# Kernel tuning notes

Measured on AMD Instinct MI355X. Metric: run time of the kernel, lower is better.

The kernel has to match this reference:

```python
import jax, jax.numpy as jnp
import numpy as np

NUM_GROUPS = 64  # matches fill_max of ids; all groups present w.h.p. so unique-inverse == ids


def setup_inputs() -> dict:
    key = jax.random.key(0)
    ks = jax.random.split(key, 8)
    B, N, D = 8, 8192, 512
    s = 1.0 / np.sqrt(D)
    return {
        "x": jax.random.normal(ks[0], (B, N, D), dtype=jnp.float32),
        "ids": jax.random.randint(ks[1], (N,), 0, NUM_GROUPS),
        "w1": jax.random.normal(ks[2], (D, D), dtype=jnp.float32) * s,
        "b1": jax.random.normal(ks[3], (D,), dtype=jnp.float32) * s,
        "w2": jax.random.normal(ks[4], (D, D), dtype=jnp.float32) * s,
        "b2": jax.random.normal(ks[5], (D,), dtype=jnp.float32) * s,
        "w3": jax.random.normal(ks[6], (D, D), dtype=jnp.float32) * s,
        "b3": jax.random.normal(ks[7], (D,), dtype=jnp.float32) * s,
    }


def reference(x, ids, w1, b1, w2, b2, w3, b3):
    # x: [B, N, D]; ids: [N] group labels in [0, NUM_GROUPS)
    G = NUM_GROUPS
    a = jnp.einsum('bnd,ed->bne', x, w1) + b1          # linear1 logits
    v = jnp.einsum('bnd,ed->bne', x, w2) + b2          # linear2 values
    # move segment axis to front: [N, B, D]
    aT = jnp.transpose(a, (1, 0, 2))
    vT = jnp.transpose(v, (1, 0, 2))
    # per-group stable softmax along the segment axis
    mx = jax.lax.stop_gradient(jax.ops.segment_max(aT, ids, num_segments=G))  # [G,B,D]
    ex = jnp.exp(aT - mx[ids])
    denom = jax.ops.segment_sum(ex, ids, num_segments=G)                      # [G,B,D]
    wts = ex / denom[ids]                                                     # [N,B,D]
    # weighted scatter-sum of values -> [G, B, D] -> [B, G, D]
    y = jnp.transpose(jax.ops.segment_sum(vT * wts, ids, num_segments=G), (1, 0, 2))
    out = jnp.einsum('bgd,ed->bge', y, w3) + b3        # linear3
    # expand: gather group outputs back to per-element rows -> [B, N, D]
    return out[:, ids]
```

## Files before the change

kernel.cpp:

```cpp
#include <hip/hip_runtime.h>
#include <hip/hip_bf16.h>
#include <math.h>

#define B_ 8
#define N_ 8192
#define D_ 512
#define G_ 64
#define M_ (B_ * N_)

typedef short bf16x8 __attribute__((ext_vector_type(8)));
typedef float f32x4 __attribute__((ext_vector_type(4)));

__device__ __forceinline__ unsigned short f2bf(float f) {
    __hip_bfloat16 h = __float2bfloat16(f);
    return *reinterpret_cast<unsigned short*>(&h);
}
__device__ __forceinline__ void gload_lds16(const void* g, void* l) {
    __builtin_amdgcn_global_load_lds((const __attribute__((address_space(1))) void*)g,
                                     (__attribute__((address_space(3))) void*)l,
                                     16, 0, 0);
}

__global__ __launch_bounds__(256) void cast_x(const float* __restrict__ x,
                                              unsigned short* __restrict__ xb) {
    size_t t = (size_t)blockIdx.x * 256 + threadIdx.x;
    float4 f = *(const float4*)(x + t * 4);
    ushort4 u;
    u.x = f2bf(f.x); u.y = f2bf(f.y); u.z = f2bf(f.z); u.w = f2bf(f.w);
    *(ushort4*)(xb + t * 4) = u;
}

__global__ __launch_bounds__(256) void cast_w(const float* __restrict__ w1,
                                              const float* __restrict__ b1,
                                              const float* __restrict__ w2,
                                              const float* __restrict__ b2,
                                              unsigned short* __restrict__ wB,
                                              float* __restrict__ biasB) {
    int t = blockIdx.x * 256 + threadIdx.x;
    int idx = t * 4;
    int row = idx >> 9;
    int col = idx & 511;
    const float* src = (row < 512) ? (w1 + (size_t)row * 512 + col)
                                   : (w2 + (size_t)(row - 512) * 512 + col);
    float4 f = *(const float4*)src;
    ushort4 u;
    u.x = f2bf(f.x); u.y = f2bf(f.y); u.z = f2bf(f.z); u.w = f2bf(f.w);
    *(ushort4*)(wB + idx) = u;
    if (t < 1024) biasB[t] = (t < 512) ? b1[t] : b2[t - 512];
}

__global__ __launch_bounds__(256) void build_lists3(const int* __restrict__ ids,
                                                    int* __restrict__ counts,
                                                    int* __restrict__ baseO,
                                                    int* __restrict__ fgO,
                                                    int* __restrict__ perm) {
    __shared__ int sid[N_];
    __shared__ unsigned short hist[256][G_];
    __shared__ int sbase[G_ + 1];
    const int t = threadIdx.x;
    for (int i = t; i < N_; i += 256) sid[i] = ids[i];
#pragma unroll
    for (int g = 0; g < G_; ++g) hist[t][g] = 0;
    __syncthreads();
    const int nb = t * 32;
    for (int k = 0; k < 32; ++k) hist[t][sid[nb + k]]++;
    __syncthreads();
    if (t < G_) {
        int run = 0;
        for (int i = 0; i < 256; ++i) {
            int v = hist[i][t];
            hist[i][t] = (unsigned short)run;
            run += v;
        }
        counts[t] = run;
    }
    __syncthreads();
    if (t == 0) {
        int acc = 0;
        for (int g = 0; g < G_; ++g) { sbase[g] = acc; acc += counts[g]; }
        sbase[G_] = acc;
    }
    __syncthreads();
    if (t < G_) baseO[t] = sbase[t];
    if (t < G_) {
        const int row = t * 128;
        int g = 0;
        while (g + 1 < G_ && sbase[g + 1] <= row) ++g;
        fgO[t] = g;
    }
    for (int k = 0; k < 32; ++k) {
        const int n = nb + k;
        const int g = sid[n];
        const int pos = sbase[g] + hist[t][g];
        hist[t][g]++;
        perm[pos] = n;
    }
}

__global__ __launch_bounds__(256) void gemm_fused(const unsigned short* __restrict__ xb,
                                                  const unsigned short* __restrict__ wB,
                                                  const float* __restrict__ biasB,
                                                  const int* __restrict__ perm,
                                                  const int* __restrict__ base,
                                                  const int* __restrict__ fg,
                                                  float* __restrict__ pt) {
    __shared__ unsigned short lsA[2][128 * 64];
    __shared__ unsigned short lsB[2][2][64 * 64];

    const int o  = blockIdx.x;
    const int mt = (o & 7) + ((o >> 6) << 3);
    const int et = (o >> 3) & 7;
    const int b  = mt >> 6;
    const int tl = mt & 63;
    const int r0 = tl * 128;

    const int tid = threadIdx.x;
    const int l = tid & 63;
    const int w = tid >> 6;
    const int wm = w >> 1, wn = w & 1;
    const int lr = l >> 3;
    const int lslot = l & 7;
    const int fr = l & 15;
    const int scol = 8 * (lslot ^ lr);

    int nrow[4];
#pragma unroll
    for (int q = 0; q < 4; ++q) nrow[q] = perm[r0 + (w * 4 + q) * 8 + lr];

    f32x4 acc_a[4][2], acc_v[4][2];
#pragma unroll
    for (int i = 0; i < 4; ++i)
#pragma unroll
        for (int j = 0; j < 2; ++j) {
            acc_a[i][j] = (f32x4){0.f, 0.f, 0.f, 0.f};
            acc_v[i][j] = (f32x4){0.f, 0.f, 0.f, 0.f};
        }

    auto stageT = [&](int buf, int kt) {
#pragma unroll
        for (int q = 0; q < 4; ++q) {
            const int c = w * 4 + q;
            gload_lds16(xb + (((size_t)(b << 13) + nrow[q]) << 9) + kt + scol,
                        &lsA[buf][c * 512]);
        }
#pragma unroll
        for (int q = 0; q < 4; ++q) {
            const int p = q >> 1;
            const int c2 = (w << 1) | (q & 1);
            const int wr = p * 512 + et * 64 + c2 * 8 + lr;
            gload_lds16(wB + ((size_t)wr << 9) + kt + scol, &lsB[buf][p][c2 * 512]);
        }
    };

    stageT(0, 0);
    __syncthreads();
    int cur = 0;
    for (int t = 0; t < 8; ++t) {
        if (t < 7) stageT(cur ^ 1, (t + 1) * 64);
#pragma unroll
        for (int ks = 0; ks < 2; ++ks) {
            const int ib = 8 * ((ks * 4 + (l >> 4)) ^ (fr & 7));
            bf16x8 af[4], bq[2][2];
#pragma unroll
            for (int i = 0; i < 4; ++i)
                af[i] = *(const bf16x8*)&lsA[cur][(wm * 64 + i * 16 + fr) * 64 + ib];
#pragma unroll
            for (int p = 0; p < 2; ++p)
#pragma unroll
                for (int j = 0; j < 2; ++j)
                    bq[p][j] = *(const bf16x8*)&lsB[cur][p][(wn * 32 + j * 16 + fr) * 64 + ib];
#pragma unroll
            for (int i = 0; i < 4; ++i)
#pragma unroll
                for (int j = 0; j < 2; ++j) {
                    acc_a[i][j] = __builtin_amdgcn_mfma_f32_16x16x32_bf16(af[i], bq[0][j], acc_a[i][j], 0, 0, 0);
                    acc_v[i][j] = __builtin_amdgcn_mfma_f32_16x16x32_bf16(af[i], bq[1][j], acc_v[i][j], 0, 0, 0);
                }
        }
        __syncthreads();
        cur ^= 1;
    }

    const int fg0 = fg[tl];
    const int bnd0 = (fg0 + 1 < G_) ? base[fg0 + 1] : (1 << 30);
    const int bnd1 = (fg0 + 2 < G_) ? base[fg0 + 2] : (1 << 30);
    const int bnd2 = (fg0 + 3 < G_) ? base[fg0 + 3] : (1 << 30);
    float b1c[2], b2c[2];
#pragma unroll
    for (int j = 0; j < 2; ++j) {
        const int col = et * 64 + wn * 32 + j * 16 + fr;
        b1c[j] = biasB[col];
        b2c[j] = biasB[512 + col];
    }
    float dpart[4][2] = {}, ypart[4][2] = {};
    const int rbase = r0 + wm * 64 + ((l >> 4) << 2);
#pragma unroll
    for (int i = 0; i < 4; ++i)
#pragma unroll
        for (int rr = 0; rr < 4; ++rr) {
            const int row = rbase + i * 16 + rr;
            const int s = (row >= bnd0) + (row >= bnd1) + (row >= bnd2);
#pragma unroll
            for (int j = 0; j < 2; ++j) {
                const float e = __expf(acc_a[i][j][rr] + b1c[j]);
                const float ey = e * (acc_v[i][j][rr] + b2c[j]);
#pragma unroll
                for (int s2 = 0; s2 < 4; ++s2) {
                    dpart[s2][j] += (s == s2) ? e : 0.f;
                    ypart[s2][j] += (s == s2) ? ey : 0.f;
                }
            }
        }
#pragma unroll
    for (int s2 = 0; s2 < 4; ++s2)
#pragma unroll
        for (int j = 0; j < 2; ++j) {
            dpart[s2][j] += __shfl_xor(dpart[s2][j], 16);
            dpart[s2][j] += __shfl_xor(dpart[s2][j], 32);
            ypart[s2][j] += __shfl_xor(ypart[s2][j], 16);
            ypart[s2][j] += __shfl_xor(ypart[s2][j], 32);
        }
    float* red = (float*)&lsA[0][0];
    if ((l >> 4) == 0) {
#pragma unroll
        for (int s2 = 0; s2 < 4; ++s2)
#pragma unroll
            for (int j = 0; j < 2; ++j) {
                const int colL = wn * 32 + j * 16 + fr;
                red[((wm * 4 + s2) * 64 + colL) * 2 + 0] = dpart[s2][j];
                red[((wm * 4 + s2) * 64 + colL) * 2 + 1] = ypart[s2][j];
            }
    }
    __syncthreads();
#pragma unroll
    for (int k = 0; k < 2; ++k) {
        const int idx = tid * 2 + k;
        const int dy = idx & 1;
        const int colL = (idx >> 1) & 63;
        const int s2 = idx >> 7;
        const float vsum = red[((0 * 4 + s2) * 64 + colL) * 2 + dy] +
                           red[((1 * 4 + s2) * 64 + colL) * 2 + dy];
        pt[((((size_t)(b * 64 + tl)) * 4 + s2) * 512 + et * 64 + colL) * 2 + dy] = vsum;
    }
}

__global__ __launch_bounds__(256) void combineC(const float* __restrict__ pt,
                                                const int* __restrict__ base,
                                                const int* __restrict__ counts,
                                                const int* __restrict__ fg,
                                                float* __restrict__ y) {
    const int g = blockIdx.x, b = blockIdx.y;
    const int bs = base[g];
    int cnt = counts[g];
    if (cnt == 0) cnt = 1;
    const int t0 = bs >> 7, t1 = (bs + cnt - 1) >> 7;
    for (int c = threadIdx.x; c < 512; c += 256) {
        float d = 0.f, yy = 0.f;
        for (int t = t0; t <= t1; ++t) {
            const int s = g - fg[t];
            if (s >= 0 && s < 4) {
                const float* p = &pt[((((size_t)(b * 64 + t)) * 4 + s) * 512 + c) * 2];
                d += p[0];
                yy += p[1];
            }
        }
        y[((size_t)(b * G_ + g)) * 512 + c] = yy / d;
    }
}

__global__ __launch_bounds__(256) void gemm3(const float* __restrict__ y,
                                             const float* __restrict__ w3,
                                             const float* __restrict__ b3,
                                             float* __restrict__ out_small) {
    __shared__ float ys[16][68];
    __shared__ float wss[16][68];
    const int m0 = blockIdx.x * 64;
    const int n0 = blockIdx.y * 64;
    const int tid = threadIdx.x;
    const int tr = tid >> 4;
    const int tc = tid & 15;
    const int lrow = tid >> 2;
    const int lk4 = (tid & 3) * 4;

    float acc[4][4] = {};

    for (int k0 = 0; k0 < D_; k0 += 16) {
        float4 yv = *(const float4*)(y + (size_t)(m0 + lrow) * D_ + k0 + lk4);
        float4 wv = *(const float4*)(w3 + (size_t)(n0 + lrow) * D_ + k0 + lk4);
        __syncthreads();
        ys[lk4 + 0][lrow] = yv.x;  ys[lk4 + 1][lrow] = yv.y;
        ys[lk4 + 2][lrow] = yv.z;  ys[lk4 + 3][lrow] = yv.w;
        wss[lk4 + 0][lrow] = wv.x; wss[lk4 + 1][lrow] = wv.y;
        wss[lk4 + 2][lrow] = wv.z; wss[lk4 + 3][lrow] = wv.w;
        __syncthreads();
#pragma unroll
        for (int kk = 0; kk < 16; ++kk) {
            float4 y4 = *(const float4*)&ys[kk][tr * 4];
            float4 w4 = *(const float4*)&wss[kk][tc * 4];
            float ya[4] = {y4.x, y4.y, y4.z, y4.w};
            float wa[4] = {w4.x, w4.y, w4.z, w4.w};
#pragma unroll
            for (int i = 0; i < 4; ++i)
#pragma unroll
                for (int j = 0; j < 4; ++j)
                    acc[i][j] = fmaf(ya[i], wa[j], acc[i][j]);
        }
    }

    float bb[4];
#pragma unroll
    for (int j = 0; j < 4; ++j) bb[j] = b3[n0 + tc * 4 + j];
#pragma unroll
    for (int i = 0; i < 4; ++i) {
        size_t o = (size_t)(m0 + tr * 4 + i) * D_ + n0 + tc * 4;
        float4 r;
        r.x = acc[i][0] + bb[0]; r.y = acc[i][1] + bb[1];
        r.z = acc[i][2] + bb[2]; r.w = acc[i][3] + bb[3];
        *(float4*)(out_small + o) = r;
    }
}

__global__ __launch_bounds__(256) void gather_out(const int* __restrict__ ids,
                                                  const float* __restrict__ out_small,
                                                  float* __restrict__ out) {
    const int c = blockIdx.x * 256 + threadIdx.x;
    const int per_row = D_ / 4;
    const int b = c / (N_ * per_row);
    const int rem = c % (N_ * per_row);
    const int n = rem / per_row;
    const int q = rem % per_row;
    const int g = ids[n];
    float4 val = *(const float4*)(out_small + ((size_t)b * G_ + g) * D_ + q * 4);
    *(float4*)(out + (size_t)c * 4) = val;
}

extern "C" void kernel_launch(void* const* d_in, const int* in_sizes, int n_in,
                              void* d_out, int out_size, void* d_ws, size_t ws_size,
                              hipStream_t stream) {
    (void)in_sizes; (void)n_in; (void)out_size; (void)ws_size;
    const float* x   = (const float*)d_in[0];
    const int*   ids = (const int*)d_in[1];
    const float* w1  = (const float*)d_in[2];
    const float* b1  = (const float*)d_in[3];
    const float* w2  = (const float*)d_in[4];
    const float* b2  = (const float*)d_in[5];
    const float* w3  = (const float*)d_in[6];
    const float* b3  = (const float*)d_in[7];
    float* out = (float*)d_out;

    float* ws_f = (float*)d_ws;
    unsigned short* xb = (unsigned short*)ws_f;
    float* after_xb  = ws_f + 16777216;
    unsigned short* wB = (unsigned short*)after_xb;
    float* biasB     = after_xb + 262144;
    float* pt        = biasB + 1024;
    float* y         = pt + 2097152;
    float* out_small = y + 262144;
    int*   perm      = (int*)(out_small + 262144);
    int*   base      = perm + N_;
    int*   counts    = base + G_;
    int*   fg        = counts + G_;

    hipLaunchKernelGGL(cast_x, dim3(32768), dim3(256), 0, stream, x, xb);
    hipLaunchKernelGGL(cast_w, dim3(512), dim3(256), 0, stream, w1, b1, w2, b2, wB, biasB);
    hipLaunchKernelGGL(build_lists3, dim3(1), dim3(256), 0, stream, ids, counts, base, fg, perm);
    hipLaunchKernelGGL(gemm_fused, dim3(4096), dim3(256), 0, stream,
                       xb, wB, biasB, perm, base, fg, pt);
    hipLaunchKernelGGL(combineC, dim3(G_, B_), dim3(256), 0, stream, pt, base, counts, fg, y);
    hipLaunchKernelGGL(gemm3, dim3(8, 8), dim3(256), 0, stream, y, w3, b3, out_small);
    hipLaunchKernelGGL(gather_out, dim3(32768), dim3(256), 0, stream, ids, out_small, out);
}
```

Before: 216.4 us.

## Fuse fp32-to-bf16 cast of x into the GEMM A-tile staging

Removes the separate cast_x kernel and its bf16 copy of x. The fused GEMM now loads fp32 rows of x into registers before the MFMA loop, converts them to bf16, and writes them to LDS after the compute for the current tile. This drops a full read and write of the 128MB activation plus a kernel launch. In exchange, the GEMM reads twice as many bytes of A per tile, uses more registers for the staging buffer, and converts in-kernel. Each x tile is also reread by the eight et column blocks, so A traffic in the GEMM grows.

```diff
diff --git a/kernel.cpp b/kernel.cpp
--- a/kernel.cpp
+++ b/kernel.cpp
@@ -19,15 +19,6 @@
     __builtin_amdgcn_global_load_lds((const __attribute__((address_space(1))) void*)g,
                                      (__attribute__((address_space(3))) void*)l,
                                      16, 0, 0);
-}
-
-__global__ __launch_bounds__(256) void cast_x(const float* __restrict__ x,
-                                              unsigned short* __restrict__ xb) {
-    size_t t = (size_t)blockIdx.x * 256 + threadIdx.x;
-    float4 f = *(const float4*)(x + t * 4);
-    ushort4 u;
-    u.x = f2bf(f.x); u.y = f2bf(f.y); u.z = f2bf(f.z); u.w = f2bf(f.w);
-    *(ushort4*)(xb + t * 4) = u;
 }
 
 __global__ __launch_bounds__(256) void cast_w(const float* __restrict__ w1,
@@ -97,7 +88,7 @@
     }
 }
 
-__global__ __launch_bounds__(256) void gemm_fused(const unsigned short* __restrict__ xb,
+__global__ __launch_bounds__(256) void gemm_fused(const float* __restrict__ x,
                                                   const unsigned short* __restrict__ wB,
                                                   const float* __restrict__ biasB,
                                                   const int* __restrict__ perm,
@@ -136,13 +127,27 @@
             acc_v[i][j] = (f32x4){0.f, 0.f, 0.f, 0.f};
         }
 
-    auto stageT = [&](int buf, int kt) {
+    float4 areg[8];
+    auto loadA = [&](int kt) {
+#pragma unroll
+        for (int q = 0; q < 4; ++q) {
+            const float* src = x + (((size_t)(b << 13) + nrow[q]) << 9) + kt + scol;
+            areg[q * 2]     = *(const float4*)src;
+            areg[q * 2 + 1] = *(const float4*)(src + 4);
+        }
+    };
+    auto writeA = [&](int buf) {
 #pragma unroll
         for (int q = 0; q < 4; ++q) {
             const int c = w * 4 + q;
-            gload_lds16(xb + (((size_t)(b << 13) + nrow[q]) << 9) + kt + scol,
-                        &lsA[buf][c * 512]);
-        }
+            union { unsigned short us[8]; uint4 v4; } pk;
+            const float* f = (const float*)&areg[q * 2];
+#pragma unroll
+            for (int e = 0; e < 8; ++e) pk.us[e] = f2bf(f[e]);
+            *(uint4*)((char*)&lsA[buf][0] + c * 1024 + l * 16) = pk.v4;
+        }
+    };
+    auto stageB = [&](int buf, int kt) {
 #pragma unroll
         for (int q = 0; q < 4; ++q) {
             const int p = q >> 1;
@@ -152,11 +157,13 @@
         }
     };
 
-    stageT(0, 0);
+    loadA(0);
+    stageB(0, 0);
+    writeA(0);
     __syncthreads();
     int cur = 0;
     for (int t = 0; t < 8; ++t) {
-        if (t < 7) stageT(cur ^ 1, (t + 1) * 64);
+        if (t < 7) { loadA((t + 1) * 64); stageB(cur ^ 1, (t + 1) * 64); }
 #pragma unroll
         for (int ks = 0; ks < 2; ++ks) {
             const int ib = 8 * ((ks * 4 + (l >> 4)) ^ (fr & 7));
@@ -177,6 +184,7 @@
                     acc_v[i][j] = __builtin_amdgcn_mfma_f32_16x16x32_bf16(af[i], bq[1][j], acc_v[i][j], 0, 0, 0);
                 }
         }
+        if (t < 7) writeA(cur ^ 1);
         __syncthreads();
         cur ^= 1;
     }
@@ -349,10 +357,8 @@
     float* out = (float*)d_out;
 
     float* ws_f = (float*)d_ws;
-    unsigned short* xb = (unsigned short*)ws_f;
-    float* after_xb  = ws_f + 16777216;
-    unsigned short* wB = (unsigned short*)after_xb;
-    float* biasB     = after_xb + 262144;
+    unsigned short* wB = (unsigned short*)ws_f;
+    float* biasB     = ws_f + 262144;
     float* pt        = biasB + 1024;
     float* y         = pt + 2097152;
     float* out_small = y + 262144;
@@ -361,11 +367,10 @@
     int*   counts    = base + G_;
     int*   fg        = counts + G_;
 
-    hipLaunchKernelGGL(cast_x, dim3(32768), dim3(256), 0, stream, x, xb);
     hipLaunchKernelGGL(cast_w, dim3(512), dim3(256), 0, stream, w1, b1, w2, b2, wB, biasB);
     hipLaunchKernelGGL(build_lists3, dim3(1), dim3(256), 0, stream, ids, counts, base, fg, perm);
     hipLaunchKernelGGL(gemm_fused, dim3(4096), dim3(256), 0, stream,
-                       xb, wB, biasB, perm, base, fg, pt);
+                       x, wB, biasB, perm, base, fg, pt);
     hipLaunchKernelGGL(combineC, dim3(G_, B_), dim3(256), 0, stream, pt, base, counts, fg, y);
     hipLaunchKernelGGL(gemm3, dim3(8, 8), dim3(256), 0, stream, y, w3, b3, out_small);
     hipLaunchKernelGGL(gather_out, dim3(32768), dim3(256), 0, stream, ids, out_small, out);
```

Result: no change. 212.3 us (-1.9%).

## Pre-permute x during bf16 cast and single-buffer GEMM LDS staging

Applied to the files above, without the earlier changes.

The cast kernel now gathers rows of x in group-sorted (perm) order while converting to bf16, so the fused GEMM reads contiguous rows instead of doing indirect per-row loads. build_lists is moved ahead of the cast so perm is ready in time. The GEMM also drops LDS double buffering, halving shared memory, which may raise occupancy but removes the overlap of the next tile's loads with the current tile's MFMAs. The cast kernel now uses a grid-stride loop over 2048 blocks and reads x through perm, so its global reads are row-gathered rather than fully sequential.

```diff
diff --git a/kernel.cpp b/kernel.cpp
--- a/kernel.cpp
+++ b/kernel.cpp
@@ -21,13 +21,22 @@
                                      16, 0, 0);
 }
 
-__global__ __launch_bounds__(256) void cast_x(const float* __restrict__ x,
-                                              unsigned short* __restrict__ xb) {
-    size_t t = (size_t)blockIdx.x * 256 + threadIdx.x;
-    float4 f = *(const float4*)(x + t * 4);
-    ushort4 u;
-    u.x = f2bf(f.x); u.y = f2bf(f.y); u.z = f2bf(f.z); u.w = f2bf(f.w);
-    *(ushort4*)(xb + t * 4) = u;
+__global__ __launch_bounds__(256) void cast_xp(const float* __restrict__ x,
+                                               const int* __restrict__ perm,
+                                               unsigned short* __restrict__ xb) {
+    const int total = M_ * 128;
+    for (int idx = blockIdx.x * 256 + threadIdx.x; idx < total;
+         idx += gridDim.x * 256) {
+        const int row = idx >> 7;
+        const int q = (idx & 127) * 4;
+        const int b = row >> 13;
+        const int i = row & 8191;
+        const float* src = x + (((size_t)(b << 13) + perm[i]) << 9) + q;
+        float4 f = *(const float4*)src;
+        ushort4 u;
+        u.x = f2bf(f.x); u.y = f2bf(f.y); u.z = f2bf(f.z); u.w = f2bf(f.w);
+        *(ushort4*)(xb + ((size_t)row << 9) + q) = u;
+    }
 }
 
 __global__ __launch_bounds__(256) void cast_w(const float* __restrict__ w1,
@@ -100,12 +109,11 @@
 __global__ __launch_bounds__(256) void gemm_fused(const unsigned short* __restrict__ xb,
                                                   const unsigned short* __restrict__ wB,
                                                   const float* __restrict__ biasB,
-                                                  const int* __restrict__ perm,
                                                   const int* __restrict__ base,
                                                   const int* __restrict__ fg,
                                                   float* __restrict__ pt) {
-    __shared__ unsigned short lsA[2][128 * 64];
-    __shared__ unsigned short lsB[2][2][64 * 64];
+    __shared__ unsigned short lsA[128 * 64];
+    __shared__ unsigned short lsB[2][64 * 64];
 
     const int o  = blockIdx.x;
     const int mt = (o & 7) + ((o >> 6) << 3);
@@ -123,10 +131,6 @@
     const int fr = l & 15;
     const int scol = 8 * (lslot ^ lr);
 
-    int nrow[4];
-#pragma unroll
-    for (int q = 0; q < 4; ++q) nrow[q] = perm[r0 + (w * 4 + q) * 8 + lr];
-
     f32x4 acc_a[4][2], acc_v[4][2];
 #pragma unroll
     for (int i = 0; i < 4; ++i)
@@ -136,39 +140,36 @@
             acc_v[i][j] = (f32x4){0.f, 0.f, 0.f, 0.f};
         }
 
-    auto stageT = [&](int buf, int kt) {
+    const size_t abase = ((size_t)(b << 13) + r0) << 9;
+
+    for (int t = 0; t < 8; ++t) {
+        const int kt = t * 64;
 #pragma unroll
         for (int q = 0; q < 4; ++q) {
             const int c = w * 4 + q;
-            gload_lds16(xb + (((size_t)(b << 13) + nrow[q]) << 9) + kt + scol,
-                        &lsA[buf][c * 512]);
+            const int row = c * 8 + lr;
+            gload_lds16(xb + abase + ((size_t)row << 9) + kt + scol, &lsA[c * 512]);
         }
 #pragma unroll
         for (int q = 0; q < 4; ++q) {
             const int p = q >> 1;
             const int c2 = (w << 1) | (q & 1);
             const int wr = p * 512 + et * 64 + c2 * 8 + lr;
-            gload_lds16(wB + ((size_t)wr << 9) + kt + scol, &lsB[buf][p][c2 * 512]);
-        }
-    };
-
-    stageT(0, 0);
-    __syncthreads();
-    int cur = 0;
-    for (int t = 0; t < 8; ++t) {
-        if (t < 7) stageT(cur ^ 1, (t + 1) * 64);
+            gload_lds16(wB + ((size_t)wr << 9) + kt + scol, &lsB[p][c2 * 512]);
+        }
+        __syncthreads();
 #pragma unroll
         for (int ks = 0; ks < 2; ++ks) {
             const int ib = 8 * ((ks * 4 + (l >> 4)) ^ (fr & 7));
             bf16x8 af[4], bq[2][2];
 #pragma unroll
             for (int i = 0; i < 4; ++i)
-                af[i] = *(const bf16x8*)&lsA[cur][(wm * 64 + i * 16 + fr) * 64 + ib];
+                af[i] = *(const bf16x8*)&lsA[(wm * 64 + i * 16 + fr) * 64 + ib];
 #pragma unroll
             for (int p = 0; p < 2; ++p)
 #pragma unroll
                 for (int j = 0; j < 2; ++j)
-                    bq[p][j] = *(const bf16x8*)&lsB[cur][p][(wn * 32 + j * 16 + fr) * 64 + ib];
+                    bq[p][j] = *(const bf16x8*)&lsB[p][(wn * 32 + j * 16 + fr) * 64 + ib];
 #pragma unroll
             for (int i = 0; i < 4; ++i)
 #pragma unroll
@@ -178,7 +179,6 @@
                 }
         }
         __syncthreads();
-        cur ^= 1;
     }
 
     const int fg0 = fg[tl];
@@ -220,7 +220,7 @@
             ypart[s2][j] += __shfl_xor(ypart[s2][j], 16);
             ypart[s2][j] += __shfl_xor(ypart[s2][j], 32);
         }
-    float* red = (float*)&lsA[0][0];
+    float* red = (float*)&lsA[0];
     if ((l >> 4) == 0) {
 #pragma unroll
         for (int s2 = 0; s2 < 4; ++s2)
@@ -361,11 +361,11 @@
     int*   counts    = base + G_;
     int*   fg        = counts + G_;
 
-    hipLaunchKernelGGL(cast_x, dim3(32768), dim3(256), 0, stream, x, xb);
+    hipLaunchKernelGGL(build_lists3, dim3(1), dim3(256), 0, stream, ids, counts, base, fg, perm);
     hipLaunchKernelGGL(cast_w, dim3(512), dim3(256), 0, stream, w1, b1, w2, b2, wB, biasB);
-    hipLaunchKernelGGL(build_lists3, dim3(1), dim3(256), 0, stream, ids, counts, base, fg, perm);
+    hipLaunchKernelGGL(cast_xp, dim3(2048), dim3(256), 0, stream, x, perm, xb);
     hipLaunchKernelGGL(gemm_fused, dim3(4096), dim3(256), 0, stream,
-                       xb, wB, biasB, perm, base, fg, pt);
+                       xb, wB, biasB, base, fg, pt);
     hipLaunchKernelGGL(combineC, dim3(G_, B_), dim3(256), 0, stream, pt, base, counts, fg, y);
     hipLaunchKernelGGL(gemm3, dim3(8, 8), dim3(256), 0, stream, y, w3, b3, out_small);
     hipLaunchKernelGGL(gather_out, dim3(32768), dim3(256), 0, stream, ids, out_small, out);
```

After: 223.2 us. 3.1% more time.
